# Kernel tuning notes

Measured on AMD Instinct MI355X. Metric: run time of the kernel, lower is better.

Reference implementation:

```python
import jax, jax.numpy as jnp
import numpy as np

EPS = 1e-5

def _bn_train(x, gamma, beta):
    # BatchNorm1d in training mode: biased batch stats over the edge dim
    mean = jnp.mean(x, axis=0)
    var = jnp.mean(jnp.square(x - mean), axis=0)
    return (x - mean) * (gamma / jnp.sqrt(var + EPS)) + beta

def setup_inputs() -> dict:
    key = jax.random.key(0)
    ks = jax.random.split(key, 12)
    E, F, G = 1000000, 64, 1024
    inp = {
        "src": jax.random.normal(ks[0], (E, F), jnp.float32),
        "dest": jax.random.normal(ks[1], (E, F), jnp.float32),
        "edge_attr": jax.random.normal(ks[2], (E, F), jnp.float32),
        "global_attr": jax.random.normal(ks[3], (G, F), jnp.float32),
        "batch": jax.random.randint(ks[4], (E,), 0, G, jnp.int64),
        # MLP params (torch Linear: y = x @ W.T + b); stored already transposed
        "W1": jax.random.normal(ks[5], (256, 64), jnp.float32) / np.sqrt(256.0),
        "b1": jnp.zeros((64,), jnp.float32),
        "W2": jax.random.normal(ks[6], (64, 64), jnp.float32) / 8.0,
        "b2": jnp.zeros((64,), jnp.float32),
        "W3": jax.random.normal(ks[7], (64, 64), jnp.float32) / 8.0,
        "b3": jnp.zeros((64,), jnp.float32),
        "g1": jnp.ones((64,), jnp.float32), "be1": jnp.zeros((64,), jnp.float32),
        "g2": jnp.ones((64,), jnp.float32), "be2": jnp.zeros((64,), jnp.float32),
        "g3": jnp.ones((64,), jnp.float32), "be3": jnp.zeros((64,), jnp.float32),
    }
    return inp

def reference(src, dest, edge_attr, global_attr, batch,
              W1, b1, W2, b2, W3, b3, g1, be1, g2, be2, g3, be3):
    # gather per-graph global attrs to edges, concat -> [E, 256]
    comb = jnp.concatenate([src, dest, edge_attr, global_attr[batch]], axis=1)
    out = _bn_train(jax.nn.relu(comb @ W1 + b1), g1, be1)
    out = _bn_train(jax.nn.relu(out @ W2 + b2), g2, be2)
    out = _bn_train(jax.nn.relu(out @ W3 + b3), g3, be3)
    # dropout p=0.0 -> identity
    return out
```

## Files before the change

kernel.cpp:

```cpp
#include <hip/hip_runtime.h>


typedef unsigned short u16;
typedef unsigned int u32;
using bf16x8 = __bf16 __attribute__((ext_vector_type(8)));
using f32x4  = float __attribute__((ext_vector_type(4)));
using u32x4  = u32 __attribute__((ext_vector_type(4)));

#define BN_EPS 1e-5f

__device__ __forceinline__ u16 f2bf(float f) {
    u32 u = __builtin_bit_cast(u32, f);
    u += 0x7fffu + ((u >> 16) & 1u);
    return (u16)(u >> 16);
}
__device__ __forceinline__ float bf2f(u16 h) {
    return __builtin_bit_cast(float, (u32)h << 16);
}
__device__ __forceinline__ u32 pk2(float a, float b) {
    return (u32)f2bf(a) | ((u32)f2bf(b) << 16);
}

__global__ __launch_bounds__(256) void prep_kernel(const float* __restrict__ W1,
                                                   u16* __restrict__ w1f,
                                                   float* __restrict__ statsz) {
    int t = blockIdx.x * 256 + threadIdx.x;
    if (t < 16384) {
        int j = t & 7, lane = (t >> 3) & 63, ct = (t >> 9) & 3, s = (t >> 11) & 1, c = t >> 12;
        int m = lane & 15, quad = lane >> 4;
        int k = c * 64 + s * 32 + quad * 8 + j;
        int n = ct * 16 + m;
        w1f[t] = f2bf(W1[k * 64 + n]);
    }
    if (t < 384) statsz[t] = 0.0f;
}

__global__ __launch_bounds__(256) void gemm1_kernel(
    const float* __restrict__ src, const float* __restrict__ dst,
    const float* __restrict__ edg, const float* __restrict__ gat,
    const int* __restrict__ batch, const u16* __restrict__ w1f,
    const float* __restrict__ b1, u16* __restrict__ Y,
    float* __restrict__ stats, int tiles)
{
    __shared__ u16 sW[16384];
    __shared__ u16 sOut[64 * 72];
    __shared__ float sSum[64], sSq[64];

    const int tid = threadIdx.x;
    {
        const u32x4* g = (const u32x4*)w1f;
        u32x4* l = (u32x4*)sW;
        #pragma unroll
        for (int i = 0; i < 8; i++) l[tid + i * 256] = g[tid + i * 256];
    }
    if (tid < 64) { sSum[tid] = 0.0f; sSq[tid] = 0.0f; }
    __syncthreads();

    const int wave = tid >> 6, lane = tid & 63;
    const int m = lane & 15, quad = lane >> 4;
    const u32x4* sWv = (const u32x4*)sW;

    float bias[4], ssum[4] = {0,0,0,0}, ssq[4] = {0,0,0,0};
    #pragma unroll
    for (int ct = 0; ct < 4; ct++) bias[ct] = b1[ct * 16 + m];

    for (int t = blockIdx.x; t < tiles; t += gridDim.x) {
        const int gr = t * 64 + wave * 16 + m;
        const float* bases[4] = { src + (size_t)gr * 64, dst + (size_t)gr * 64,
                                  edg + (size_t)gr * 64, gat + (size_t)batch[gr] * 64 };
        f32x4 acc[4] = {{0,0,0,0},{0,0,0,0},{0,0,0,0},{0,0,0,0}};
        #pragma unroll
        for (int c = 0; c < 4; c++) {
            const float* p = bases[c] + quad * 8;
            #pragma unroll
            for (int s = 0; s < 2; s++) {
                float4 f0 = *(const float4*)(p + s * 32);
                float4 f1 = *(const float4*)(p + s * 32 + 4);
                u32x4 av = { pk2(f0.x, f0.y), pk2(f0.z, f0.w),
                             pk2(f1.x, f1.y), pk2(f1.z, f1.w) };
                bf16x8 af = __builtin_bit_cast(bf16x8, av);
                #pragma unroll
                for (int ct = 0; ct < 4; ct++) {
                    bf16x8 bf = __builtin_bit_cast(bf16x8, sWv[((c * 2 + s) * 4 + ct) * 64 + lane]);
                    acc[ct] = __builtin_amdgcn_mfma_f32_16x16x32_bf16(af, bf, acc[ct], 0, 0, 0);
                }
            }
        }
        #pragma unroll
        for (int ct = 0; ct < 4; ct++) {
            #pragma unroll
            for (int r = 0; r < 4; r++) {
                float x = fmaxf(acc[ct][r] + bias[ct], 0.0f);
                ssum[ct] += x;
                ssq[ct] = fmaf(x, x, ssq[ct]);
                sOut[(wave * 16 + quad * 4 + r) * 72 + ct * 16 + m] = f2bf(x);
            }
        }
        __syncthreads();
        {
            u16* yt = Y + (size_t)t * 4096;
            #pragma unroll
            for (int p = 0; p < 2; p++) {
                int id = tid + p * 256;
                u32x4 v = *(const u32x4*)(sOut + (id >> 3) * 72 + (id & 7) * 8);
                *(u32x4*)(yt + id * 8) = v;
            }
        }
        __syncthreads();
    }
    #pragma unroll
    for (int ct = 0; ct < 4; ct++) {
        float s = ssum[ct], q = ssq[ct];
        s += __shfl_xor(s, 16); s += __shfl_xor(s, 32);
        q += __shfl_xor(q, 16); q += __shfl_xor(q, 32);
        if (lane < 16) { atomicAdd(&sSum[ct * 16 + lane], s); atomicAdd(&sSq[ct * 16 + lane], q); }
    }
    __syncthreads();
    if (tid < 64) { atomicAdd(&stats[tid], sSum[tid]); atomicAdd(&stats[64 + tid], sSq[tid]); }
}

__global__ void fin_fold_kernel(const float* __restrict__ stats, float invE,
                                const float* __restrict__ g, const float* __restrict__ be,
                                const float* __restrict__ W, const float* __restrict__ b,
                                u16* __restrict__ wt_out, float* __restrict__ b_out)
{
    int n = threadIdx.x;
    float bacc = b[n];
    for (int k = 0; k < 64; k++) {
        float mean = stats[k] * invE;
        float var  = stats[64 + k] * invE - mean * mean;
        float a = g[k] / sqrtf(var + BN_EPS);
        float c = be[k] - mean * a;
        float w = W[k * 64 + n];
        wt_out[n * 64 + k] = f2bf(a * w);
        bacc = fmaf(c, w, bacc);
    }
    b_out[n] = bacc;
}

__global__ void fin_affine_kernel(const float* __restrict__ stats, float invE,
                                  const float* __restrict__ g, const float* __restrict__ be,
                                  float* __restrict__ a_out, float* __restrict__ c_out)
{
    int n = threadIdx.x;
    float mean = stats[n] * invE;
    float var  = stats[64 + n] * invE - mean * mean;
    float a = g[n] / sqrtf(var + BN_EPS);
    a_out[n] = a;
    c_out[n] = be[n] - mean * a;
}

template<int WF32>
__global__ __launch_bounds__(256) void gemm64_kernel(
    const u16* __restrict__ X, const u16* __restrict__ Wt,
    const float* __restrict__ bias_in, u16* __restrict__ Ybf,
    float* __restrict__ Yf, float* __restrict__ stats, int tiles)
{
    __shared__ u16 sOut[64 * 72];
    __shared__ float sSum[64], sSq[64];
    const int tid = threadIdx.x;
    if (tid < 64) { sSum[tid] = 0.0f; sSq[tid] = 0.0f; }
    __syncthreads();
    const int wave = tid >> 6, lane = tid & 63;
    const int m = lane & 15, quad = lane >> 4;

    bf16x8 Bf[2][4];
    #pragma unroll
    for (int s = 0; s < 2; s++)
        #pragma unroll
        for (int ct = 0; ct < 4; ct++)
            Bf[s][ct] = __builtin_bit_cast(bf16x8,
                *(const u32x4*)(Wt + (ct * 16 + m) * 64 + s * 32 + quad * 8));

    float bias[4], ssum[4] = {0,0,0,0}, ssq[4] = {0,0,0,0};
    #pragma unroll
    for (int ct = 0; ct < 4; ct++) bias[ct] = bias_in[ct * 16 + m];

    for (int t = blockIdx.x; t < tiles; t += gridDim.x) {
        const u16* xp = X + (size_t)(t * 64 + wave * 16 + m) * 64 + quad * 8;
        f32x4 acc[4] = {{0,0,0,0},{0,0,0,0},{0,0,0,0},{0,0,0,0}};
        #pragma unroll
        for (int s = 0; s < 2; s++) {
            bf16x8 af = __builtin_bit_cast(bf16x8, *(const u32x4*)(xp + s * 32));
            #pragma unroll
            for (int ct = 0; ct < 4; ct++)
                acc[ct] = __builtin_amdgcn_mfma_f32_16x16x32_bf16(af, Bf[s][ct], acc[ct], 0, 0, 0);
        }
        #pragma unroll
        for (int ct = 0; ct < 4; ct++) {
            #pragma unroll
            for (int r = 0; r < 4; r++) {
                float x = fmaxf(acc[ct][r] + bias[ct], 0.0f);
                ssum[ct] += x;
                ssq[ct] = fmaf(x, x, ssq[ct]);
                if (WF32)
                    Yf[(size_t)(t * 64 + wave * 16 + quad * 4 + r) * 64 + ct * 16 + m] = x;
                else
                    sOut[(wave * 16 + quad * 4 + r) * 72 + ct * 16 + m] = f2bf(x);
            }
        }
        if (!WF32) {
            __syncthreads();
            u16* yt = Ybf + (size_t)t * 4096;
            #pragma unroll
            for (int p = 0; p < 2; p++) {
                int id = tid + p * 256;
                u32x4 v = *(const u32x4*)(sOut + (id >> 3) * 72 + (id & 7) * 8);
                *(u32x4*)(yt + id * 8) = v;
            }
            __syncthreads();
        }
    }
    #pragma unroll
    for (int ct = 0; ct < 4; ct++) {
        float s = ssum[ct], q = ssq[ct];
        s += __shfl_xor(s, 16); s += __shfl_xor(s, 32);
        q += __shfl_xor(q, 16); q += __shfl_xor(q, 32);
        if (lane < 16) { atomicAdd(&sSum[ct * 16 + lane], s); atomicAdd(&sSq[ct * 16 + lane], q); }
    }
    __syncthreads();
    if (tid < 64) { atomicAdd(&stats[tid], sSum[tid]); atomicAdd(&stats[64 + tid], sSq[tid]); }
}

__global__ __launch_bounds__(256) void bn_apply_bf_kernel(const u16* __restrict__ X,
    const float* __restrict__ a3, const float* __restrict__ c3,
    float* __restrict__ out, int nchunk)
{
    int t0 = blockIdx.x * 256 + threadIdx.x;
    int colb = (t0 & 7) * 8;
    float a[8], c[8];
    #pragma unroll
    for (int i = 0; i < 8; i++) { a[i] = a3[colb + i]; c[i] = c3[colb + i]; }
    int stride = gridDim.x * 256;
    for (int t = t0; t < nchunk; t += stride) {
        u32x4 v = *(const u32x4*)(X + (size_t)t * 8);
        float4 o0, o1;
        o0.x = fmaf(a[0], bf2f((u16)(v.x & 0xffffu)), c[0]);
        o0.y = fmaf(a[1], bf2f((u16)(v.x >> 16)),     c[1]);
        o0.z = fmaf(a[2], bf2f((u16)(v.y & 0xffffu)), c[2]);
        o0.w = fmaf(a[3], bf2f((u16)(v.y >> 16)),     c[3]);
        o1.x = fmaf(a[4], bf2f((u16)(v.z & 0xffffu)), c[4]);
        o1.y = fmaf(a[5], bf2f((u16)(v.z >> 16)),     c[5]);
        o1.z = fmaf(a[6], bf2f((u16)(v.w & 0xffffu)), c[6]);
        o1.w = fmaf(a[7], bf2f((u16)(v.w >> 16)),     c[7]);
        *(float4*)(out + (size_t)t * 8)     = o0;
        *(float4*)(out + (size_t)t * 8 + 4) = o1;
    }
}

__global__ __launch_bounds__(256) void bn_apply_f32_kernel(float* __restrict__ Y,
    const float* __restrict__ a3, const float* __restrict__ c3, int nchunk)
{
    int t0 = blockIdx.x * 256 + threadIdx.x;
    int colb = (t0 & 7) * 8;
    float a[8], c[8];
    #pragma unroll
    for (int i = 0; i < 8; i++) { a[i] = a3[colb + i]; c[i] = c3[colb + i]; }
    int stride = gridDim.x * 256;
    for (int t = t0; t < nchunk; t += stride) {
        float4 x0 = *(const float4*)(Y + (size_t)t * 8);
        float4 x1 = *(const float4*)(Y + (size_t)t * 8 + 4);
        x0.x = fmaf(a[0], x0.x, c[0]); x0.y = fmaf(a[1], x0.y, c[1]);
        x0.z = fmaf(a[2], x0.z, c[2]); x0.w = fmaf(a[3], x0.w, c[3]);
        x1.x = fmaf(a[4], x1.x, c[4]); x1.y = fmaf(a[5], x1.y, c[5]);
        x1.z = fmaf(a[6], x1.z, c[6]); x1.w = fmaf(a[7], x1.w, c[7]);
        *(float4*)(Y + (size_t)t * 8)     = x0;
        *(float4*)(Y + (size_t)t * 8 + 4) = x1;
    }
}

extern "C" void kernel_launch(void* const* d_in, const int* in_sizes, int n_in,
                              void* d_out, int out_size, void* d_ws, size_t ws_size,
                              hipStream_t stream)
{
    const float* src  = (const float*)d_in[0];
    const float* dst  = (const float*)d_in[1];
    const float* edg  = (const float*)d_in[2];
    const float* gat  = (const float*)d_in[3];
    const int*   batch= (const int*)d_in[4];
    const float* W1 = (const float*)d_in[5];
    const float* b1 = (const float*)d_in[6];
    const float* W2 = (const float*)d_in[7];
    const float* b2 = (const float*)d_in[8];
    const float* W3 = (const float*)d_in[9];
    const float* b3 = (const float*)d_in[10];
    const float* g1 = (const float*)d_in[11];
    const float* be1= (const float*)d_in[12];
    const float* g2 = (const float*)d_in[13];
    const float* be2= (const float*)d_in[14];
    const float* g3 = (const float*)d_in[15];
    const float* be3= (const float*)d_in[16];

    const int E = in_sizes[0] / 64;
    const int tiles = E / 64;
    const float invE = 1.0f / (float)E;

    char* ws = (char*)d_ws;
    u16*   w1f = (u16*)(ws + 0);
    u16*   w2t = (u16*)(ws + 36864);
    u16*   w3t = (u16*)(ws + 45056);
    float* b2p = (float*)(ws + 53248);
    float* b3p = (float*)(ws + 53504);
    float* st1 = (float*)(ws + 53760);
    float* st2 = (float*)(ws + 54272);
    float* st3 = (float*)(ws + 54784);
    float* a3  = (float*)(ws + 55296);
    float* c3  = (float*)(ws + 55552);

    const size_t OFF_H = 65536;
    const size_t HSZ = (size_t)E * 128;

    u16* h1 = (u16*)(ws + OFF_H);
    u16* h2; u16* h3 = nullptr; bool f32out;
    if (ws_size >= OFF_H + 3 * HSZ) {
        h2 = (u16*)(ws + OFF_H + HSZ); h3 = (u16*)(ws + OFF_H + 2 * HSZ); f32out = false;
    } else if (ws_size >= OFF_H + 2 * HSZ) {
        h2 = (u16*)(ws + OFF_H + HSZ); f32out = true;
    } else {
        h2 = (u16*)d_out; h3 = h1; f32out = false;
    }

    prep_kernel<<<64, 256, 0, stream>>>(W1, w1f, st1);
    gemm1_kernel<<<1536, 256, 0, stream>>>(src, dst, edg, gat, batch, w1f, b1, h1, st1, tiles);
    fin_fold_kernel<<<1, 64, 0, stream>>>(st1, invE, g1, be1, W2, b2, w2t, b2p);
    gemm64_kernel<0><<<1536, 256, 0, stream>>>(h1, w2t, b2p, h2, nullptr, st2, tiles);
    fin_fold_kernel<<<1, 64, 0, stream>>>(st2, invE, g2, be2, W3, b3, w3t, b3p);
    if (!f32out) {
        gemm64_kernel<0><<<1536, 256, 0, stream>>>(h2, w3t, b3p, h3, nullptr, st3, tiles);
        fin_affine_kernel<<<1, 64, 0, stream>>>(st3, invE, g3, be3, a3, c3);
        bn_apply_bf_kernel<<<4096, 256, 0, stream>>>(h3, a3, c3, (float*)d_out, E * 8);
    } else {
        gemm64_kernel<1><<<1536, 256, 0, stream>>>(h2, w3t, b3p, nullptr, (float*)d_out, st3, tiles);
        fin_affine_kernel<<<1, 64, 0, stream>>>(st3, invE, g3, be3, a3, c3);
        bn_apply_f32_kernel<<<4096, 256, 0, stream>>>((float*)d_out, a3, c3, E * 8);
    }
}
```

Baseline: 1.004 ms.

## Fuse BN folding into GEMMs and recompute layer three to skip intermediate writes

Folds the BatchNorm statistics-to-weight folding into each 64x64 GEMM kernel's preamble, which removes the separate tiny fold and affine launches. Layer three now runs twice: a stats-only pass that writes nothing, then a pass that recomputes the GEMM and applies the final BN affine while writing fp32 output directly. This drops the h3 buffer and the separate bn_apply pass. It also gives each wave a private LDS staging buffer in place of the block-wide __syncthreads, switches the 64x64 kernels to per-wave tiles with the loads hoisted ahead of the MFMAs, and prefetches the next batch index in gemm1. The cost is a second read of h2 and a redundant GEMM, and every block re-derives the folded weights.

```diff
diff --git a/kernel.cpp b/kernel.cpp
--- a/kernel.cpp
+++ b/kernel.cpp
@@ -13,9 +13,6 @@
     u32 u = __builtin_bit_cast(u32, f);
     u += 0x7fffu + ((u >> 16) & 1u);
     return (u16)(u >> 16);
-}
-__device__ __forceinline__ float bf2f(u16 h) {
-    return __builtin_bit_cast(float, (u32)h << 16);
 }
 __device__ __forceinline__ u32 pk2(float a, float b) {
     return (u32)f2bf(a) | ((u32)f2bf(b) << 16);
@@ -43,9 +40,8 @@
     float* __restrict__ stats, int tiles)
 {
     __shared__ u16 sW[16384];
-    __shared__ u16 sOut[64 * 72];
+    __shared__ u16 sOut[4][1152];
     __shared__ float sSum[64], sSq[64];
-
     const int tid = threadIdx.x;
     {
         const u32x4* g = (const u32x4*)w1f;
@@ -53,29 +49,50 @@
         #pragma unroll
         for (int i = 0; i < 8; i++) l[tid + i * 256] = g[tid + i * 256];
     }
-    if (tid < 64) { sSum[tid] = 0.0f; sSq[tid] = 0.0f; }
+    if (tid < 64) { sSum[tid] = 0.f; sSq[tid] = 0.f; }
     __syncthreads();
 
     const int wave = tid >> 6, lane = tid & 63;
     const int m = lane & 15, quad = lane >> 4;
     const u32x4* sWv = (const u32x4*)sW;
-
-    float bias[4], ssum[4] = {0,0,0,0}, ssq[4] = {0,0,0,0};
+    u16* so = sOut[wave];
+
+    float bias[4];
     #pragma unroll
     for (int ct = 0; ct < 4; ct++) bias[ct] = b1[ct * 16 + m];
-
-    for (int t = blockIdx.x; t < tiles; t += gridDim.x) {
-        const int gr = t * 64 + wave * 16 + m;
-        const float* bases[4] = { src + (size_t)gr * 64, dst + (size_t)gr * 64,
-                                  edg + (size_t)gr * 64, gat + (size_t)batch[gr] * 64 };
+    float ssum[4] = {0,0,0,0}, ssq[4] = {0,0,0,0};
+
+    const int gs = gridDim.x;
+    const int rowoff = wave * 16 + m;
+    int t = blockIdx.x;
+    int bi = (t < tiles) ? batch[(size_t)t * 64 + rowoff] : 0;
+
+    for (; t < tiles; t += gs) {
+        const size_t rbase = (size_t)t * 64 + wave * 16;
+        float4 L[16];
+        {
+            const float* p0 = src + (rbase + m) * 64 + quad * 8;
+            const float* p1 = dst + (rbase + m) * 64 + quad * 8;
+            const float* p2 = edg + (rbase + m) * 64 + quad * 8;
+            const float* p3 = gat + (size_t)bi * 64 + quad * 8;
+            L[0]  = *(const float4*)(p0);      L[1]  = *(const float4*)(p0 + 4);
+            L[2]  = *(const float4*)(p0 + 32); L[3]  = *(const float4*)(p0 + 36);
+            L[4]  = *(const float4*)(p1);      L[5]  = *(const float4*)(p1 + 4);
+            L[6]  = *(const float4*)(p1 + 32); L[7]  = *(const float4*)(p1 + 36);
+            L[8]  = *(const float4*)(p2);      L[9]  = *(const float4*)(p2 + 4);
+            L[10] = *(const float4*)(p2 + 32); L[11] = *(const float4*)(p2 + 36);
+            L[12] = *(const float4*)(p3);      L[13] = *(const float4*)(p3 + 4);
+            L[14] = *(const float4*)(p3 + 32); L[15] = *(const float4*)(p3 + 36);
+        }
+        int tn = t + gs;
+        int bn = (tn < tiles) ? batch[(size_t)tn * 64 + rowoff] : 0;
+
         f32x4 acc[4] = {{0,0,0,0},{0,0,0,0},{0,0,0,0},{0,0,0,0}};
         #pragma unroll
         for (int c = 0; c < 4; c++) {
-            const float* p = bases[c] + quad * 8;
             #pragma unroll
             for (int s = 0; s < 2; s++) {
-                float4 f0 = *(const float4*)(p + s * 32);
-                float4 f1 = *(const float4*)(p + s * 32 + 4);
+                float4 f0 = L[c * 4 + s * 2], f1 = L[c * 4 + s * 2 + 1];
                 u32x4 av = { pk2(f0.x, f0.y), pk2(f0.z, f0.w),
                              pk2(f1.x, f1.y), pk2(f1.z, f1.w) };
                 bf16x8 af = __builtin_bit_cast(bf16x8, av);
@@ -90,23 +107,22 @@
         for (int ct = 0; ct < 4; ct++) {
             #pragma unroll
             for (int r = 0; r < 4; r++) {
-                float x = fmaxf(acc[ct][r] + bias[ct], 0.0f);
-                ssum[ct] += x;
-                ssq[ct] = fmaf(x, x, ssq[ct]);
-                sOut[(wave * 16 + quad * 4 + r) * 72 + ct * 16 + m] = f2bf(x);
-            }
-        }
-        __syncthreads();
+                float x = fmaxf(acc[ct][r] + bias[ct], 0.f);
+                ssum[ct] += x; ssq[ct] = fmaf(x, x, ssq[ct]);
+                so[(quad * 4 + r) * 72 + ct * 16 + m] = f2bf(x);
+            }
+        }
+        __threadfence_block();
         {
-            u16* yt = Y + (size_t)t * 4096;
-            #pragma unroll
-            for (int p = 0; p < 2; p++) {
-                int id = tid + p * 256;
-                u32x4 v = *(const u32x4*)(sOut + (id >> 3) * 72 + (id & 7) * 8);
-                *(u32x4*)(yt + id * 8) = v;
-            }
-        }
-        __syncthreads();
+            int row = lane >> 2, seg = lane & 3;
+            const u16* rp = so + row * 72 + seg * 16;
+            u32x4 v0 = *(const u32x4*)rp;
+            u32x4 v1 = *(const u32x4*)(rp + 8);
+            u16* yp = Y + (rbase + row) * 64 + seg * 16;
+            *(u32x4*)yp = v0;
+            *(u32x4*)(yp + 8) = v1;
+        }
+        bi = bn;
     }
     #pragma unroll
     for (int ct = 0; ct < 4; ct++) {
@@ -119,96 +135,99 @@
     if (tid < 64) { atomicAdd(&stats[tid], sSum[tid]); atomicAdd(&stats[64 + tid], sSq[tid]); }
 }
 
-__global__ void fin_fold_kernel(const float* __restrict__ stats, float invE,
-                                const float* __restrict__ g, const float* __restrict__ be,
-                                const float* __restrict__ W, const float* __restrict__ b,
-                                u16* __restrict__ wt_out, float* __restrict__ b_out)
+#define FOLD_PREAMBLE(STATS, G, BE, W, B)                                      \
+    for (int i = tid; i < 1024; i += 256)                                      \
+        ((float4*)sWf)[i] = ((const float4*)(W))[i];                           \
+    if (tid < 64) {                                                            \
+        float mean = (STATS)[tid] * invE;                                      \
+        float var  = (STATS)[64 + tid] * invE - mean * mean;                   \
+        float a = (G)[tid] / sqrtf(var + BN_EPS);                              \
+        sAc[tid] = a; sCc[tid] = (BE)[tid] - mean * a;                         \
+        sSum[tid] = 0.f; sSq[tid] = 0.f;                                       \
+    }                                                                          \
+    __syncthreads();                                                           \
+    if (tid < 64) {                                                            \
+        float bacc = (B)[tid];                                                 \
+        for (int k = 0; k < 64; k++) bacc = fmaf(sCc[k], sWf[k * 64 + tid], bacc); \
+        sBp[tid] = bacc;                                                       \
+    }                                                                          \
+    __syncthreads();                                                           \
+    bf16x8 Bf[2][4];                                                           \
+    float bias[4];                                                             \
+    {                                                                          \
+        _Pragma("unroll")                                                      \
+        for (int s = 0; s < 2; s++) {                                          \
+            _Pragma("unroll")                                                  \
+            for (int ct = 0; ct < 4; ct++) {                                   \
+                int n = ct * 16 + m;                                           \
+                u32x4 wv;                                                      \
+                _Pragma("unroll")                                              \
+                for (int jj = 0; jj < 4; jj++) {                               \
+                    int k = s * 32 + quad * 8 + jj * 2;                        \
+                    wv[jj] = pk2(sAc[k] * sWf[k * 64 + n],                     \
+                                 sAc[k + 1] * sWf[(k + 1) * 64 + n]);          \
+                }                                                              \
+                Bf[s][ct] = __builtin_bit_cast(bf16x8, wv);                    \
+            }                                                                  \
+        }                                                                      \
+        _Pragma("unroll")                                                      \
+        for (int ct = 0; ct < 4; ct++) bias[ct] = sBp[ct * 16 + m];            \
+    }
+
+__global__ __launch_bounds__(256) void gemm_mid_kernel(
+    const u16* __restrict__ X, const float* __restrict__ W, const float* __restrict__ b,
+    const float* __restrict__ stats_in, float invE,
+    const float* __restrict__ g, const float* __restrict__ be,
+    u16* __restrict__ Y, float* __restrict__ stats_out, int tiles)
 {
-    int n = threadIdx.x;
-    float bacc = b[n];
-    for (int k = 0; k < 64; k++) {
-        float mean = stats[k] * invE;
-        float var  = stats[64 + k] * invE - mean * mean;
-        float a = g[k] / sqrtf(var + BN_EPS);
-        float c = be[k] - mean * a;
-        float w = W[k * 64 + n];
-        wt_out[n * 64 + k] = f2bf(a * w);
-        bacc = fmaf(c, w, bacc);
-    }
-    b_out[n] = bacc;
-}
-
-__global__ void fin_affine_kernel(const float* __restrict__ stats, float invE,
-                                  const float* __restrict__ g, const float* __restrict__ be,
-                                  float* __restrict__ a_out, float* __restrict__ c_out)
-{
-    int n = threadIdx.x;
-    float mean = stats[n] * invE;
-    float var  = stats[64 + n] * invE - mean * mean;
-    float a = g[n] / sqrtf(var + BN_EPS);
-    a_out[n] = a;
-    c_out[n] = be[n] - mean * a;
-}
-
-template<int WF32>
-__global__ __launch_bounds__(256) void gemm64_kernel(
-    const u16* __restrict__ X, const u16* __restrict__ Wt,
-    const float* __restrict__ bias_in, u16* __restrict__ Ybf,
-    float* __restrict__ Yf, float* __restrict__ stats, int tiles)
-{
-    __shared__ u16 sOut[64 * 72];
+    __shared__ float sWf[4096];
+    __shared__ float sAc[64], sCc[64], sBp[64];
     __shared__ float sSum[64], sSq[64];
+    __shared__ u16 sOut[4][1152];
     const int tid = threadIdx.x;
-    if (tid < 64) { sSum[tid] = 0.0f; sSq[tid] = 0.0f; }
-    __syncthreads();
     const int wave = tid >> 6, lane = tid & 63;
     const int m = lane & 15, quad = lane >> 4;
 
-    bf16x8 Bf[2][4];
-    #pragma unroll
-    for (int s = 0; s < 2; s++)
-        #pragma unroll
-        for (int ct = 0; ct < 4; ct++)
-            Bf[s][ct] = __builtin_bit_cast(bf16x8,
-                *(const u32x4*)(Wt + (ct * 16 + m) * 64 + s * 32 + quad * 8));
-
-    float bias[4], ssum[4] = {0,0,0,0}, ssq[4] = {0,0,0,0};
-    #pragma unroll
-    for (int ct = 0; ct < 4; ct++) bias[ct] = bias_in[ct * 16 + m];
-
-    for (int t = blockIdx.x; t < tiles; t += gridDim.x) {
-        const u16* xp = X + (size_t)(t * 64 + wave * 16 + m) * 64 + quad * 8;
-        f32x4 acc[4] = {{0,0,0,0},{0,0,0,0},{0,0,0,0},{0,0,0,0}};
-        #pragma unroll
-        for (int s = 0; s < 2; s++) {
-            bf16x8 af = __builtin_bit_cast(bf16x8, *(const u32x4*)(xp + s * 32));
-            #pragma unroll
-            for (int ct = 0; ct < 4; ct++)
-                acc[ct] = __builtin_amdgcn_mfma_f32_16x16x32_bf16(af, Bf[s][ct], acc[ct], 0, 0, 0);
-        }
-        #pragma unroll
-        for (int ct = 0; ct < 4; ct++) {
-            #pragma unroll
-            for (int r = 0; r < 4; r++) {
-                float x = fmaxf(acc[ct][r] + bias[ct], 0.0f);
-                ssum[ct] += x;
-                ssq[ct] = fmaf(x, x, ssq[ct]);
-                if (WF32)
-                    Yf[(size_t)(t * 64 + wave * 16 + quad * 4 + r) * 64 + ct * 16 + m] = x;
-                else
-                    sOut[(wave * 16 + quad * 4 + r) * 72 + ct * 16 + m] = f2bf(x);
-            }
-        }
-        if (!WF32) {
-            __syncthreads();
-            u16* yt = Ybf + (size_t)t * 4096;
-            #pragma unroll
-            for (int p = 0; p < 2; p++) {
-                int id = tid + p * 256;
-                u32x4 v = *(const u32x4*)(sOut + (id >> 3) * 72 + (id & 7) * 8);
-                *(u32x4*)(yt + id * 8) = v;
-            }
-            __syncthreads();
+    FOLD_PREAMBLE(stats_in, g, be, W, b)
+
+    float ssum[4] = {0,0,0,0}, ssq[4] = {0,0,0,0};
+    u16* so = sOut[wave];
+    const int nw = gridDim.x * 4;
+    for (int t = blockIdx.x * 4 + wave; t < tiles; t += nw) {
+        u32x4 Xf[8];
+        const u16* xb = X + (size_t)t * 4096 + m * 64 + quad * 8;
+        #pragma unroll
+        for (int u = 0; u < 4; u++) {
+            Xf[u * 2]     = *(const u32x4*)(xb + u * 1024);
+            Xf[u * 2 + 1] = *(const u32x4*)(xb + u * 1024 + 32);
+        }
+        #pragma unroll
+        for (int u = 0; u < 4; u++) {
+            f32x4 acc[4] = {{0,0,0,0},{0,0,0,0},{0,0,0,0},{0,0,0,0}};
+            #pragma unroll
+            for (int s = 0; s < 2; s++) {
+                bf16x8 af = __builtin_bit_cast(bf16x8, Xf[u * 2 + s]);
+                #pragma unroll
+                for (int ct = 0; ct < 4; ct++)
+                    acc[ct] = __builtin_amdgcn_mfma_f32_16x16x32_bf16(af, Bf[s][ct], acc[ct], 0, 0, 0);
+            }
+            #pragma unroll
+            for (int ct = 0; ct < 4; ct++) {
+                #pragma unroll
+                for (int r = 0; r < 4; r++) {
+                    float x = fmaxf(acc[ct][r] + bias[ct], 0.f);
+                    ssum[ct] += x; ssq[ct] = fmaf(x, x, ssq[ct]);
+                    so[(quad * 4 + r) * 72 + ct * 16 + m] = f2bf(x);
+                }
+            }
+            __threadfence_block();
+            int row = lane >> 2, seg = lane & 3;
+            const u16* rp = so + row * 72 + seg * 16;
+            u32x4 v0 = *(const u32x4*)rp;
+            u32x4 v1 = *(const u32x4*)(rp + 8);
+            u16* yp = Y + (size_t)t * 4096 + (u * 16 + row) * 64 + seg * 16;
+            *(u32x4*)yp = v0;
+            *(u32x4*)(yp + 8) = v1;
         }
     }
     #pragma unroll
@@ -219,54 +238,136 @@
         if (lane < 16) { atomicAdd(&sSum[ct * 16 + lane], s); atomicAdd(&sSq[ct * 16 + lane], q); }
     }
     __syncthreads();
-    if (tid < 64) { atomicAdd(&stats[tid], sSum[tid]); atomicAdd(&stats[64 + tid], sSq[tid]); }
-}
-
-__global__ __launch_bounds__(256) void bn_apply_bf_kernel(const u16* __restrict__ X,
-    const float* __restrict__ a3, const float* __restrict__ c3,
-    float* __restrict__ out, int nchunk)
+    if (tid < 64) { atomicAdd(&stats_out[tid], sSum[tid]); atomicAdd(&stats_out[64 + tid], sSq[tid]); }
+}
+
+__global__ __launch_bounds__(256) void gemm_stats_kernel(
+    const u16* __restrict__ X, const float* __restrict__ W, const float* __restrict__ b,
+    const float* __restrict__ stats_in, float invE,
+    const float* __restrict__ g, const float* __restrict__ be,
+    float* __restrict__ stats_out, int tiles)
 {
-    int t0 = blockIdx.x * 256 + threadIdx.x;
-    int colb = (t0 & 7) * 8;
-    float a[8], c[8];
+    __shared__ float sWf[4096];
+    __shared__ float sAc[64], sCc[64], sBp[64];
+    __shared__ float sSum[64], sSq[64];
+    const int tid = threadIdx.x;
+    const int wave = tid >> 6, lane = tid & 63;
+    const int m = lane & 15, quad = lane >> 4;
+
+    FOLD_PREAMBLE(stats_in, g, be, W, b)
+
+    float ssum[4] = {0,0,0,0}, ssq[4] = {0,0,0,0};
+    const int nw = gridDim.x * 4;
+    for (int t = blockIdx.x * 4 + wave; t < tiles; t += nw) {
+        u32x4 Xf[8];
+        const u16* xb = X + (size_t)t * 4096 + m * 64 + quad * 8;
+        #pragma unroll
+        for (int u = 0; u < 4; u++) {
+            Xf[u * 2]     = *(const u32x4*)(xb + u * 1024);
+            Xf[u * 2 + 1] = *(const u32x4*)(xb + u * 1024 + 32);
+        }
+        #pragma unroll
+        for (int u = 0; u < 4; u++) {
+            f32x4 acc[4] = {{0,0,0,0},{0,0,0,0},{0,0,0,0},{0,0,0,0}};
+            #pragma unroll
+            for (int s = 0; s < 2; s++) {
+                bf16x8 af = __builtin_bit_cast(bf16x8, Xf[u * 2 + s]);
+                #pragma unroll
+                for (int ct = 0; ct < 4; ct++)
+                    acc[ct] = __builtin_amdgcn_mfma_f32_16x16x32_bf16(af, Bf[s][ct], acc[ct], 0, 0, 0);
+            }
+            #pragma unroll
+            for (int ct = 0; ct < 4; ct++) {
+                #pragma unroll
+                for (int r = 0; r < 4; r++) {
+                    float x = fmaxf(acc[ct][r] + bias[ct], 0.f);
+                    ssum[ct] += x; ssq[ct] = fmaf(x, x, ssq[ct]);
+                }
+            }
+        }
+    }
     #pragma unroll
-    for (int i = 0; i < 8; i++) { a[i] = a3[colb + i]; c[i] = c3[colb + i]; }
-    int stride = gridDim.x * 256;
-    for (int t = t0; t < nchunk; t += stride) {
-        u32x4 v = *(const u32x4*)(X + (size_t)t * 8);
-        float4 o0, o1;
-        o0.x = fmaf(a[0], bf2f((u16)(v.x & 0xffffu)), c[0]);
-        o0.y = fmaf(a[1], bf2f((u16)(v.x >> 16)),     c[1]);
-        o0.z = fmaf(a[2], bf2f((u16)(v.y & 0xffffu)), c[2]);
-        o0.w = fmaf(a[3], bf2f((u16)(v.y >> 16)),     c[3]);
-        o1.x = fmaf(a[4], bf2f((u16)(v.z & 0xffffu)), c[4]);
-        o1.y = fmaf(a[5], bf2f((u16)(v.z >> 16)),     c[5]);
-        o1.z = fmaf(a[6], bf2f((u16)(v.w & 0xffffu)), c[6]);
-        o1.w = fmaf(a[7], bf2f((u16)(v.w >> 16)),     c[7]);
-        *(float4*)(out + (size_t)t * 8)     = o0;
-        *(float4*)(out + (size_t)t * 8 + 4) = o1;
-    }
-}
-
-__global__ __launch_bounds__(256) void bn_apply_f32_kernel(float* __restrict__ Y,
-    const float* __restrict__ a3, const float* __restrict__ c3, int nchunk)
+    for (int ct = 0; ct < 4; ct++) {
+        float s = ssum[ct], q = ssq[ct];
+        s += __shfl_xor(s, 16); s += __shfl_xor(s, 32);
+        q += __shfl_xor(q, 16); q += __shfl_xor(q, 32);
+        if (lane < 16) { atomicAdd(&sSum[ct * 16 + lane], s); atomicAdd(&sSq[ct * 16 + lane], q); }
+    }
+    __syncthreads();
+    if (tid < 64) { atomicAdd(&stats_out[tid], sSum[tid]); atomicAdd(&stats_out[64 + tid], sSq[tid]); }
+}
+
+__global__ __launch_bounds__(256) void gemm_out_kernel(
+    const u16* __restrict__ X, const float* __restrict__ W, const float* __restrict__ b,
+    const float* __restrict__ stats_in, float invE,
+    const float* __restrict__ g, const float* __restrict__ be,
+    const float* __restrict__ stats3, const float* __restrict__ g3,
+    const float* __restrict__ be3, float* __restrict__ out, int tiles)
 {
-    int t0 = blockIdx.x * 256 + threadIdx.x;
-    int colb = (t0 & 7) * 8;
-    float a[8], c[8];
+    __shared__ float sWf[4096];
+    __shared__ float sAc[64], sCc[64], sBp[64];
+    __shared__ float sSum[64], sSq[64];
+    __shared__ float sA3[64], sC3[64];
+    __shared__ float sOutF[4][1088];
+    const int tid = threadIdx.x;
+    const int wave = tid >> 6, lane = tid & 63;
+    const int m = lane & 15, quad = lane >> 4;
+
+    if (tid < 64) {
+        float mean = stats3[tid] * invE;
+        float var  = stats3[64 + tid] * invE - mean * mean;
+        float a = g3[tid] / sqrtf(var + BN_EPS);
+        sA3[tid] = a; sC3[tid] = be3[tid] - mean * a;
+    }
+    FOLD_PREAMBLE(stats_in, g, be, W, b)
+
+    float a3r[4], c3r[4];
     #pragma unroll
-    for (int i = 0; i < 8; i++) { a[i] = a3[colb + i]; c[i] = c3[colb + i]; }
-    int stride = gridDim.x * 256;
-    for (int t = t0; t < nchunk; t += stride) {
-        float4 x0 = *(const float4*)(Y + (size_t)t * 8);
-        float4 x1 = *(const float4*)(Y + (size_t)t * 8 + 4);
-        x0.x = fmaf(a[0], x0.x, c[0]); x0.y = fmaf(a[1], x0.y, c[1]);
-        x0.z = fmaf(a[2], x0.z, c[2]); x0.w = fmaf(a[3], x0.w, c[3]);
-        x1.x = fmaf(a[4], x1.x, c[4]); x1.y = fmaf(a[5], x1.y, c[5]);
-        x1.z = fmaf(a[6], x1.z, c[6]); x1.w = fmaf(a[7], x1.w, c[7]);
-        *(float4*)(Y + (size_t)t * 8)     = x0;
-        *(float4*)(Y + (size_t)t * 8 + 4) = x1;
-    }
+    for (int ct = 0; ct < 4; ct++) { a3r[ct] = sA3[ct * 16 + m]; c3r[ct] = sC3[ct * 16 + m]; }
+
+    float* sof = sOutF[wave];
+    const int nw = gridDim.x * 4;
+    for (int t = blockIdx.x * 4 + wave; t < tiles; t += nw) {
+        u32x4 Xf[8];
+        const u16* xb = X + (size_t)t * 4096 + m * 64 + quad * 8;
+        #pragma unroll
+        for (int u = 0; u < 4; u++) {
+            Xf[u * 2]     = *(const u32x4*)(xb + u * 1024);
+            Xf[u * 2 + 1] = *(const u32x4*)(xb + u * 1024 + 32);
+        }
+        #pragma unroll
+        for (int u = 0; u < 4; u++) {
+            f32x4 acc[4] = {{0,0,0,0},{0,0,0,0},{0,0,0,0},{0,0,0,0}};
+            #pragma unroll
+            for (int s = 0; s < 2; s++) {
+                bf16x8 af = __builtin_bit_cast(bf16x8, Xf[u * 2 + s]);
+                #pragma unroll
+                for (int ct = 0; ct < 4; ct++)
+                    acc[ct] = __builtin_amdgcn_mfma_f32_16x16x32_bf16(af, Bf[s][ct], acc[ct], 0, 0, 0);
+            }
+            #pragma unroll
+            for (int ct = 0; ct < 4; ct++) {
+                #pragma unroll
+                for (int r = 0; r < 4; r++) {
+                    float x = fmaxf(acc[ct][r] + bias[ct], 0.f);
+                    sof[(quad * 4 + r) * 68 + ct * 16 + m] = fmaf(a3r[ct], x, c3r[ct]);
+                }
+            }
+            __threadfence_block();
+            int row = lane >> 2, seg = lane & 3;
+            const float* rp = sof + row * 68 + seg * 16;
+            float4 v0 = *(const float4*)rp;
+            float4 v1 = *(const float4*)(rp + 4);
+            float4 v2 = *(const float4*)(rp + 8);
+            float4 v3 = *(const float4*)(rp + 12);
+            float* op = out + ((size_t)t * 64 + u * 16 + row) * 64 + seg * 16;
+            *(float4*)op       = v0;
+            *(float4*)(op + 4) = v1;
+            *(float4*)(op + 8) = v2;
+            *(float4*)(op + 12) = v3;
+        }
+    }
+    (void)sSum; (void)sSq;
 }
 
 extern "C" void kernel_launch(void* const* d_in, const int* in_sizes, int n_in,
@@ -297,41 +398,23 @@
 
     char* ws = (char*)d_ws;
     u16*   w1f = (u16*)(ws + 0);
-    u16*   w2t = (u16*)(ws + 36864);
-    u16*   w3t = (u16*)(ws + 45056);
-    float* b2p = (float*)(ws + 53248);
-    float* b3p = (float*)(ws + 53504);
-    float* st1 = (float*)(ws + 53760);
-    float* st2 = (float*)(ws + 54272);
-    float* st3 = (float*)(ws + 54784);
-    float* a3  = (float*)(ws + 55296);
-    float* c3  = (float*)(ws + 55552);
+    float* st1 = (float*)(ws + 49152);
+    float* st2 = st1 + 128;
+    float* st3 = st1 + 256;
 
     const size_t OFF_H = 65536;
     const size_t HSZ = (size_t)E * 128;
-
-    u16* h1 = (u16*)(ws + OFF_H);
-    u16* h2; u16* h3 = nullptr; bool f32out;
-    if (ws_size >= OFF_H + 3 * HSZ) {
-        h2 = (u16*)(ws + OFF_H + HSZ); h3 = (u16*)(ws + OFF_H + 2 * HSZ); f32out = false;
-    } else if (ws_size >= OFF_H + 2 * HSZ) {
-        h2 = (u16*)(ws + OFF_H + HSZ); f32out = true;
+    u16 *h1, *h2;
+    if (ws_size >= OFF_H + 2 * HSZ) {
+        h1 = (u16*)(ws + OFF_H); h2 = (u16*)(ws + OFF_H + HSZ);
     } else {
-        h2 = (u16*)d_out; h3 = h1; f32out = false;
+        h1 = (u16*)d_out; h2 = (u16*)(ws + OFF_H);
     }
 
     prep_kernel<<<64, 256, 0, stream>>>(W1, w1f, st1);
     gemm1_kernel<<<1536, 256, 0, stream>>>(src, dst, edg, gat, batch, w1f, b1, h1, st1, tiles);
-    fin_fold_kernel<<<1, 64, 0, stream>>>(st1, invE, g1, be1, W2, b2, w2t, b2p);
-    gemm64_kernel<0><<<1536, 256, 0, stream>>>(h1, w2t, b2p, h2, nullptr, st2, tiles);
-    fin_fold_kernel<<<1, 64, 0, stream>>>(st2, invE, g2, be2, W3, b3, w3t, b3p);
-    if (!f32out) {
-        gemm64_kernel<0><<<1536, 256, 0, stream>>>(h2, w3t, b3p, h3, nullptr, st3, tiles);
-        fin_affine_kernel<<<1, 64, 0, stream>>>(st3, invE, g3, be3, a3, c3);
-        bn_apply_bf_kernel<<<4096, 256, 0, stream>>>(h3, a3, c3, (float*)d_out, E * 8);
-    } else {
-        gemm64_kernel<1><<<1536, 256, 0, stream>>>(h2, w3t, b3p, nullptr, (float*)d_out, st3, tiles);
-        fin_affine_kernel<<<1, 64, 0, stream>>>(st3, invE, g3, be3, a3, c3);
-        bn_apply_f32_kernel<<<4096, 256, 0, stream>>>((float*)d_out, a3, c3, E * 8);
-    }
-}
+    gemm_mid_kernel<<<1024, 256, 0, stream>>>(h1, W2, b2, st1, invE, g1, be1, h2, st2, tiles);
+    gemm_stats_kernel<<<1024, 256, 0, stream>>>(h2, W3, b3, st2, invE, g2, be2, st3, tiles);
+    gemm_out_kernel<<<1024, 256, 0, stream>>>(h2, W3, b3, st2, invE, g2, be2, st3, g3, be3,
+                                              (float*)d_out, tiles);
+}
```

Result: faster. 938.6 us (-6.5%).
